# Kernel optimization log

Measured on AMD Instinct MI355X. Metric: run time of the kernel, lower is better.

Reference implementation:

```python
import jax, jax.numpy as jnp
import numpy as np

N, C, H, W = 16, 64, 256, 256
M_BUCKETS = 128  # min(H*W/144, 128) saturates at 128 for H=W=256


def setup_inputs() -> dict:
    key = jax.random.key(0)
    k1, k2 = jax.random.split(key)
    inputs = jax.random.normal(k1, (N, C, H, W), dtype=jnp.float32)
    # LSH random-projection matrices, one per batch element: (N, C, m)
    random_matrices = jax.random.normal(k2, (N, C, M_BUCKETS), dtype=jnp.float32)
    return {"inputs": inputs, "random_matrices": random_matrices}


def reference(inputs, random_matrices):
    n, c, h, w = inputs.shape
    # Flatten spatial dims: each of the H*W pixels has a C-dim feature vector.
    x = inputs.reshape(n, c, h * w)  # (N, C, P) with P = H*W
    # Per-pixel hash logits via random projection: (N, P, m)
    hash_code = jnp.einsum('ncp,ncm->npm', x, random_matrices)
    return hash_code
```

## Files before the change

kernel.cpp:

```cpp
#include <hip/hip_runtime.h>


#define NB   16
#define CDIM 64
#define PDIM 65536
#define MDIM 128
#define PT   128
#define BLOCKS_PER_N 64
#define TILES_PER_BLOCK 8
#define XS   132

typedef __attribute__((ext_vector_type(8))) short bf16x8;
typedef __attribute__((ext_vector_type(4))) float f32x4;

__device__ __forceinline__ unsigned short f2bf(float f) {
  union { float f; unsigned int u; } v; v.f = f;
  unsigned int u = v.u;
  u += 0x7fffu + ((u >> 16) & 1u);
  return (unsigned short)(u >> 16);
}

__device__ __forceinline__ int swz(int row, int col) {
  int slot = (col >> 3) ^ (row & 7);
  return row * 64 + slot * 8 + (col & 7);
}

__global__ __launch_bounds__(256, 4) void nlsa_kernel(
    const float* __restrict__ x, const float* __restrict__ rm,
    float* __restrict__ out) {
  __shared__ unsigned short lds_rm[MDIM * CDIM];
  __shared__ unsigned short lds_x[CDIM * XS];

  const int t = threadIdx.x;
  const int b = blockIdx.x;
  const int n  = b >> 6;
  const int bt = b & 63;

  const float* xn   = x  + (size_t)n * CDIM * PDIM;
  const float* rmn  = rm + (size_t)n * CDIM * MDIM;
  float*       outn = out + (size_t)n * PDIM * MDIM;

  const int cst = t >> 5;
  const int pst = (t & 31) * 4;

  float4 r[8];
  {
    const float* src = xn + (size_t)(bt * PT + pst);
#pragma unroll
    for (int it = 0; it < 8; ++it)
      r[it] = *(const float4*)(src + (size_t)(cst + it * 8) * PDIM);
  }

  {
    const int m  = t & 127;
    const int cb = (t >> 7) * 4;
#pragma unroll
    for (int it = 0; it < 8; ++it) {
      const int c0 = cb + it * 8;
      ushort4 v;
      v.x = f2bf(rmn[(c0 + 0) * MDIM + m]);
      v.y = f2bf(rmn[(c0 + 1) * MDIM + m]);
      v.z = f2bf(rmn[(c0 + 2) * MDIM + m]);
      v.w = f2bf(rmn[(c0 + 3) * MDIM + m]);
      *(ushort4*)&lds_rm[swz(m, c0)] = v;
    }
  }
  __syncthreads();

  const int w  = t >> 6;
  const int l  = t & 63;
  const int lo = l & 15;
  const int g  = l >> 4;

  bf16x8 a[2][2];
#pragma unroll
  for (int mt = 0; mt < 2; ++mt)
#pragma unroll
    for (int ks = 0; ks < 2; ++ks)
      a[mt][ks] = *(const bf16x8*)&lds_rm[swz(w * 32 + mt * 16 + lo,
                                              ks * 32 + g * 8)];

  for (int k = 0; k < TILES_PER_BLOCK; ++k) {
    asm volatile("" ::: "memory");
    __builtin_amdgcn_s_barrier();
    asm volatile("" ::: "memory");

#pragma unroll
    for (int it = 0; it < 8; ++it) {
      ushort4 v;
      v.x = f2bf(r[it].x); v.y = f2bf(r[it].y);
      v.z = f2bf(r[it].z); v.w = f2bf(r[it].w);
      *(ushort4*)&lds_x[(cst + it * 8) * XS + pst] = v;
    }

    if (k + 1 < TILES_PER_BLOCK) {
      const float* src = xn + (size_t)((bt + (k + 1) * BLOCKS_PER_N) * PT + pst);
#pragma unroll
      for (int it = 0; it < 8; ++it)
        r[it] = *(const float4*)(src + (size_t)(cst + it * 8) * PDIM);
    }

    asm volatile("s_waitcnt lgkmcnt(0)" ::: "memory");
    __builtin_amdgcn_s_barrier();
    asm volatile("" ::: "memory");

    const int p_base = (bt + k * BLOCKS_PER_N) * PT;
#pragma unroll
    for (int pt_ = 0; pt_ < 8; ++pt_) {
      const int pl = pt_ * 16 + lo;
      bf16x8 b0, b1;
#pragma unroll
      for (int i = 0; i < 8; ++i) {
        b0[i] = (short)lds_x[(g * 8 + i) * XS + pl];
        b1[i] = (short)lds_x[(32 + g * 8 + i) * XS + pl];
      }
      f32x4 acc0 = {0.f, 0.f, 0.f, 0.f};
      f32x4 acc1 = {0.f, 0.f, 0.f, 0.f};
      acc0 = __builtin_amdgcn_mfma_f32_16x16x32_bf16(a[0][0], b0, acc0, 0, 0, 0);
      acc0 = __builtin_amdgcn_mfma_f32_16x16x32_bf16(a[0][1], b1, acc0, 0, 0, 0);
      acc1 = __builtin_amdgcn_mfma_f32_16x16x32_bf16(a[1][0], b0, acc1, 0, 0, 0);
      acc1 = __builtin_amdgcn_mfma_f32_16x16x32_bf16(a[1][1], b1, acc1, 0, 0, 0);

      float* dst = outn + (size_t)(p_base + pl) * MDIM + w * 32 + g * 4;
      *(f32x4*)(dst)      = acc0;
      *(f32x4*)(dst + 16) = acc1;
    }
  }
}

extern "C" void kernel_launch(void* const* d_in, const int* in_sizes, int n_in,
                              void* d_out, int out_size, void* d_ws, size_t ws_size,
                              hipStream_t stream) {
  const float* x  = (const float*)d_in[0];
  const float* rm = (const float*)d_in[1];
  float* out = (float*)d_out;
  nlsa_kernel<<<dim3(NB * BLOCKS_PER_N), dim3(256), 0, stream>>>(x, rm, out);
}
```

Baseline: 161.7 us.

## Double-buffer x tile in LDS, swizzle columns, use nontemporal output stores

Reuses the rm staging area as a second x buffer so the next tile is converted and written to LDS while the current tile is consumed by MFMA. This leaves one barrier per iteration instead of two. It also XOR-swizzles the x tile columns by channel group to reduce LDS bank conflicts on the strided b-fragment reads. Output stores become nontemporal to avoid polluting cache with the write-only 512MB result. The cost is more register pressure from the overlapping load/convert and more complex indexing.

```diff
diff --git a/kernel.cpp b/kernel.cpp
--- a/kernel.cpp
+++ b/kernel.cpp
@@ -7,7 +7,7 @@
 #define MDIM 128
 #define PT   128
 #define BLOCKS_PER_N 64
-#define TILES_PER_BLOCK 8
+#define TILES 8
 #define XS   132
 
 typedef __attribute__((ext_vector_type(8))) short bf16x8;
@@ -25,11 +25,14 @@
   return row * 64 + slot * 8 + (col & 7);
 }
 
+__device__ __forceinline__ int xswz(int c, int p) {
+  return c * XS + (p ^ (((c >> 3) & 3) << 4));
+}
+
 __global__ __launch_bounds__(256, 4) void nlsa_kernel(
     const float* __restrict__ x, const float* __restrict__ rm,
     float* __restrict__ out) {
-  __shared__ unsigned short lds_rm[MDIM * CDIM];
-  __shared__ unsigned short lds_x[CDIM * XS];
+  __shared__ unsigned short lds[2][CDIM * XS];
 
   const int t = threadIdx.x;
   const int b = blockIdx.x;
@@ -62,7 +65,7 @@
       v.y = f2bf(rmn[(c0 + 1) * MDIM + m]);
       v.z = f2bf(rmn[(c0 + 2) * MDIM + m]);
       v.w = f2bf(rmn[(c0 + 3) * MDIM + m]);
-      *(ushort4*)&lds_rm[swz(m, c0)] = v;
+      *(ushort4*)&lds[1][swz(m, c0)] = v;
     }
   }
   __syncthreads();
@@ -77,42 +80,58 @@
   for (int mt = 0; mt < 2; ++mt)
 #pragma unroll
     for (int ks = 0; ks < 2; ++ks)
-      a[mt][ks] = *(const bf16x8*)&lds_rm[swz(w * 32 + mt * 16 + lo,
+      a[mt][ks] = *(const bf16x8*)&lds[1][swz(w * 32 + mt * 16 + lo,
                                               ks * 32 + g * 8)];
 
-  for (int k = 0; k < TILES_PER_BLOCK; ++k) {
-    asm volatile("" ::: "memory");
-    __builtin_amdgcn_s_barrier();
-    asm volatile("" ::: "memory");
+#pragma unroll
+  for (int it = 0; it < 8; ++it) {
+    ushort4 v;
+    v.x = f2bf(r[it].x); v.y = f2bf(r[it].y);
+    v.z = f2bf(r[it].z); v.w = f2bf(r[it].w);
+    *(ushort4*)&lds[0][xswz(cst + it * 8, pst)] = v;
+  }
+  {
+    const float* src = xn + (size_t)((bt + BLOCKS_PER_N) * PT + pst);
+#pragma unroll
+    for (int it = 0; it < 8; ++it)
+      r[it] = *(const float4*)(src + (size_t)(cst + it * 8) * PDIM);
+  }
 
+  asm volatile("s_waitcnt lgkmcnt(0)" ::: "memory");
+  __builtin_amdgcn_s_barrier();
+  asm volatile("" ::: "memory");
+
+  for (int k = 0; k < TILES; ++k) {
+    unsigned short* cur = lds[k & 1];
+    unsigned short* nxt = lds[(k + 1) & 1];
+
+    if (k + 1 < TILES) {
 #pragma unroll
-    for (int it = 0; it < 8; ++it) {
-      ushort4 v;
-      v.x = f2bf(r[it].x); v.y = f2bf(r[it].y);
-      v.z = f2bf(r[it].z); v.w = f2bf(r[it].w);
-      *(ushort4*)&lds_x[(cst + it * 8) * XS + pst] = v;
+      for (int it = 0; it < 8; ++it) {
+        ushort4 v;
+        v.x = f2bf(r[it].x); v.y = f2bf(r[it].y);
+        v.z = f2bf(r[it].z); v.w = f2bf(r[it].w);
+        *(ushort4*)&nxt[xswz(cst + it * 8, pst)] = v;
+      }
+      if (k + 2 < TILES) {
+        const float* src =
+            xn + (size_t)((bt + (k + 2) * BLOCKS_PER_N) * PT + pst);
+#pragma unroll
+        for (int it = 0; it < 8; ++it)
+          r[it] = *(const float4*)(src + (size_t)(cst + it * 8) * PDIM);
+      }
     }
-
-    if (k + 1 < TILES_PER_BLOCK) {
-      const float* src = xn + (size_t)((bt + (k + 1) * BLOCKS_PER_N) * PT + pst);
-#pragma unroll
-      for (int it = 0; it < 8; ++it)
-        r[it] = *(const float4*)(src + (size_t)(cst + it * 8) * PDIM);
-    }
-
-    asm volatile("s_waitcnt lgkmcnt(0)" ::: "memory");
-    __builtin_amdgcn_s_barrier();
-    asm volatile("" ::: "memory");
 
     const int p_base = (bt + k * BLOCKS_PER_N) * PT;
 #pragma unroll
     for (int pt_ = 0; pt_ < 8; ++pt_) {
-      const int pl = pt_ * 16 + lo;
+      const int pl  = pt_ * 16 + lo;
+      const int pls = pl ^ (g << 4);
       bf16x8 b0, b1;
 #pragma unroll
       for (int i = 0; i < 8; ++i) {
-        b0[i] = (short)lds_x[(g * 8 + i) * XS + pl];
-        b1[i] = (short)lds_x[(32 + g * 8 + i) * XS + pl];
+        b0[i] = (short)cur[(g * 8 + i) * XS + pls];
+        b1[i] = (short)cur[(32 + g * 8 + i) * XS + pls];
       }
       f32x4 acc0 = {0.f, 0.f, 0.f, 0.f};
       f32x4 acc1 = {0.f, 0.f, 0.f, 0.f};
@@ -122,9 +141,13 @@
       acc1 = __builtin_amdgcn_mfma_f32_16x16x32_bf16(a[1][1], b1, acc1, 0, 0, 0);
 
       float* dst = outn + (size_t)(p_base + pl) * MDIM + w * 32 + g * 4;
-      *(f32x4*)(dst)      = acc0;
-      *(f32x4*)(dst + 16) = acc1;
+      __builtin_nontemporal_store(acc0, (f32x4*)(dst));
+      __builtin_nontemporal_store(acc1, (f32x4*)(dst + 16));
     }
+
+    asm volatile("s_waitcnt lgkmcnt(0)" ::: "memory");
+    __builtin_amdgcn_s_barrier();
+    asm volatile("" ::: "memory");
   }
 }
 
```

New measurement: 176.8 us. 9.4% more time.
